# Performance work log

Hardware: AMD Instinct MI355X
Metric: run time of the kernel (lower is better)

## Reference

```python
import jax, jax.numpy as jnp
import numpy as np

N_NODES = 50000
N_EDGES = 400000
IN_DIM = 64
HID = 128
HEADS = 4
NEG_SLOPE = 0.2


def gat_conv(x, src, dst, W, a_src, a_dst, b, heads, out_ch, concat):
    N = x.shape[0]
    h = (x @ W).reshape(N, heads, out_ch)                 # [N,H,C]
    alpha_s = jnp.einsum('nhc,hc->nh', h, a_src)          # [N,H]
    alpha_d = jnp.einsum('nhc,hc->nh', h, a_dst)
    e = jax.nn.leaky_relu(alpha_s[src] + alpha_d[dst], NEG_SLOPE)  # [E,H]
    m = jax.ops.segment_max(e, dst, num_segments=N)
    m = jnp.where(jnp.isfinite(m), m, 0.0)
    ex = jnp.exp(e - m[dst])
    s = jax.ops.segment_sum(ex, dst, num_segments=N)
    alpha = ex / s[dst]                                   # segment softmax over incoming edges
    out = jax.ops.segment_sum(h[src] * alpha[:, :, None], dst, num_segments=N)  # [N,H,C]
    out = out.reshape(N, heads * out_ch) if concat else out.mean(axis=1)
    return out + b


def setup_inputs() -> dict:
    key = jax.random.key(0)
    ks = jax.random.split(key, 20)
    g = lambda i, shape, sc: (jax.random.normal(ks[i], shape, jnp.float32) * sc)
    x = g(0, (N_NODES, IN_DIM), 1.0)
    edge_index = jax.random.randint(ks[1], (2, N_EDGES), 0, N_NODES, dtype=jnp.int32)
    d = {
        'x': x, 'edge_index': edge_index,
        'W1': g(2, (IN_DIM, HEADS * HID), 0.1), 'a_src1': g(3, (HEADS, HID), 0.1), 'a_dst1': g(4, (HEADS, HID), 0.1), 'b1': jnp.zeros((HEADS * HID,), jnp.float32),
        'W2': g(5, (HEADS * HID, HEADS * HID), 0.05), 'a_src2': g(6, (HEADS, HID), 0.1), 'a_dst2': g(7, (HEADS, HID), 0.1), 'b2': jnp.zeros((HEADS * HID,), jnp.float32),
        'W3': g(8, (HEADS * HID, HID), 0.05), 'a_src3': g(9, (1, HID), 0.1), 'a_dst3': g(10, (1, HID), 0.1), 'b3': jnp.zeros((HID,), jnp.float32),
        'fc1_w': g(11, (HID, HID // 2), 0.1), 'fc1_b': jnp.zeros((HID // 2,), jnp.float32),
        'fc2_w': g(12, (HID // 2, 1), 0.1), 'fc2_b': jnp.zeros((1,), jnp.float32),
    }
    return d


def reference(x, edge_index, W1, a_src1, a_dst1, b1, W2, a_src2, a_dst2, b2, W3, a_src3, a_dst3, b3, fc1_w, fc1_b, fc2_w, fc2_b):
    N = x.shape[0]
    loop = jnp.arange(N, dtype=edge_index.dtype)
    src = jnp.concatenate([edge_index[0], loop])  # PyG GATConv adds self-loops by default
    dst = jnp.concatenate([edge_index[1], loop])
    h = jax.nn.elu(gat_conv(x, src, dst, W1, a_src1, a_dst1, b1, HEADS, HID, True))
    h = jax.nn.elu(gat_conv(h, src, dst, W2, a_src2, a_dst2, b2, HEADS, HID, True))
    h = jax.nn.elu(gat_conv(h, src, dst, W3, a_src3, a_dst3, b3, 1, HID, False))
    h = jax.nn.relu(h @ fc1_w + fc1_b)
    return jax.nn.sigmoid(h @ fc2_w + fc2_b)  # [N, 1]
```

## Files before the change

kernel.cpp:

```cpp
#include <hip/hip_runtime.h>
#include <math.h>

typedef __attribute__((ext_vector_type(8))) short short8;
typedef __attribute__((ext_vector_type(4))) float f32x4;
typedef unsigned short u16;
typedef unsigned int u32;

__device__ inline u16 f2b(float f) {
  u32 u = __float_as_uint(f);
  return (u16)((u + 0x7FFFu + ((u >> 16) & 1u)) >> 16);
}
__device__ inline float b2f(u16 b) { return __uint_as_float((u32)b << 16); }
__device__ inline float lrelu(float v) { return v > 0.f ? v : 0.2f * v; }
__device__ inline float elu1(float v) { return v > 0.f ? v : __expf(v) - 1.f; }

__device__ inline void gld_lds16(const void* g, void* l) {
  __builtin_amdgcn_global_load_lds((const __attribute__((address_space(1))) void*)g,
                                   (__attribute__((address_space(3))) void*)l, 16, 0, 0);
}

__global__ void fused_prep(const float* __restrict__ W1, u16* __restrict__ Wt1,
                           const float* __restrict__ W2, u16* __restrict__ Wt2,
                           const float* __restrict__ W3, u16* __restrict__ Wt3,
                           const int* __restrict__ ei, int E0, int ET,
                           int* __restrict__ deg) {
  int i = blockIdx.x * blockDim.x + threadIdx.x;
  if (i < 64 * 512) {
    int k = i / 512, n = i % 512;
    Wt1[n * 64 + k] = f2b(W1[i]);
    return;
  }
  i -= 64 * 512;
  if (i < 512 * 512) {
    int k = i / 512, n = i % 512;
    Wt2[n * 512 + k] = f2b(W2[i]);
    return;
  }
  i -= 512 * 512;
  if (i < 512 * 128) {
    int k = i / 128, n = i % 128;
    Wt3[n * 512 + k] = f2b(W3[i]);
    return;
  }
  i -= 512 * 128;
  if (i < ET) {
    int d = (i < E0) ? ei[E0 + i] : (i - E0);
    atomicAdd(&deg[d], 1);
  }
}

__global__ __launch_bounds__(256) void gemm_bf16_gat(
    const u16* __restrict__ A, const u16* __restrict__ Bt, u16* __restrict__ Hb,
    const float* __restrict__ a_src, const float* __restrict__ a_dst,
    float* __restrict__ aS, float* __restrict__ aD, int M, int HC, int K, int Hh,
    int gy, int nStrips) {
  int mIdx, nIdx;
  if (nStrips == 4) {
    int l = blockIdx.x;
    int xcd = l & 7, k = l >> 3;
    nIdx = k & 3;
    mIdx = xcd + 8 * (k >> 2);
    if (mIdx >= gy) return;
  } else {
    mIdx = blockIdx.x;
    nIdx = 0;
  }
  __shared__ u16 As[128 * 32];
  __shared__ u16 Bs[128 * 32];
  __shared__ float sRed[2][2][128];
  const int tid = threadIdx.x;
  const int w = tid >> 6, lane = tid & 63;
  const int wm = w >> 1, wn = w & 1;
  const int q = lane >> 4, l15 = lane & 15;
  const int nBase = nIdx * 128;
  const int mBase = mIdx * 128;
  const int h = nBase >> 7;
  const int srow = lane >> 2;
  const int skc = (lane & 3) * 8;

  f32x4 acc[4][4];
#pragma unroll
  for (int i = 0; i < 4; ++i)
#pragma unroll
    for (int j = 0; j < 4; ++j) acc[i][j] = (f32x4){0.f, 0.f, 0.f, 0.f};

  for (int k0 = 0; k0 < K; k0 += 32) {
#pragma unroll
    for (int r = 0; r < 2; ++r) {
      int lrow = w * 32 + r * 16 + srow;
      int ga = mBase + lrow;
      if (ga >= M) ga = M - 1;
      gld_lds16(A + (size_t)ga * K + k0 + skc, &As[(w * 32 + r * 16) * 32]);
      int gb = nBase + lrow;
      gld_lds16(Bt + (size_t)gb * K + k0 + skc, &Bs[(w * 32 + r * 16) * 32]);
    }
    __syncthreads();
    short8 af[4], bf[4];
#pragma unroll
    for (int i = 0; i < 4; ++i)
      af[i] = *(const short8*)&As[(wm * 64 + i * 16 + l15) * 32 + q * 8];
#pragma unroll
    for (int j = 0; j < 4; ++j)
      bf[j] = *(const short8*)&Bs[(wn * 64 + j * 16 + l15) * 32 + q * 8];
#pragma unroll
    for (int i = 0; i < 4; ++i)
#pragma unroll
      for (int j = 0; j < 4; ++j)
        acc[i][j] = __builtin_amdgcn_mfma_f32_16x16x32_bf16(af[i], bf[j], acc[i][j], 0, 0, 0);
    __syncthreads();
  }

  float asv[4], adv[4];
#pragma unroll
  for (int j = 0; j < 4; ++j) {
    int cw = wn * 64 + j * 16 + l15;
    asv[j] = a_src[h * 128 + cw];
    adv[j] = a_dst[h * 128 + cw];
  }
#pragma unroll
  for (int mi = 0; mi < 4; ++mi) {
#pragma unroll
    for (int r = 0; r < 4; ++r) {
      int row = mBase + wm * 64 + mi * 16 + q * 4 + r;
      float s = 0.f, d = 0.f;
#pragma unroll
      for (int j = 0; j < 4; ++j) {
        float v = acc[mi][j][r];
        s = fmaf(v, asv[j], s);
        d = fmaf(v, adv[j], d);
        if (row < M) Hb[(size_t)row * HC + nBase + wn * 64 + j * 16 + l15] = f2b(v);
      }
#pragma unroll
      for (int o = 8; o; o >>= 1) {
        s += __shfl_xor(s, o);
        d += __shfl_xor(d, o);
      }
      if (l15 == 0) {
        int lr = wm * 64 + mi * 16 + q * 4 + r;
        sRed[0][wn][lr] = s;
        sRed[1][wn][lr] = d;
      }
    }
  }
  __syncthreads();
  if (tid < 128) {
    int row = mBase + tid;
    if (row < M) {
      aS[(size_t)row * Hh + h] = sRed[0][0][tid] + sRed[0][1][tid];
      aD[(size_t)row * Hh + h] = sRed[1][0][tid] + sRed[1][1][tid];
    }
  }
}

__global__ __launch_bounds__(256) void gemm_bd_l1(
    const u16* __restrict__ A, const u16* __restrict__ Bt,
    const float* __restrict__ bias, u16* __restrict__ outB, int M, int gy) {
  int l = blockIdx.x;
  int xcd = l & 7, kk = l >> 3;
  int nIdx = kk & 3;
  int mIdx = xcd + 8 * (kk >> 2);
  if (mIdx >= gy) return;
  __shared__ u16 As[128 * 32];
  __shared__ u16 Bs[128 * 32];
  const int tid = threadIdx.x;
  const int w = tid >> 6, lane = tid & 63;
  const int wm = w >> 1, wn = w & 1;
  const int q = lane >> 4, l15 = lane & 15;
  const int nBase = nIdx * 128, mBase = mIdx * 128;
  const int srow = lane >> 2, skc = (lane & 3) * 8;

  f32x4 acc[4][4];
#pragma unroll
  for (int i = 0; i < 4; ++i)
#pragma unroll
    for (int j = 0; j < 4; ++j) acc[i][j] = (f32x4){0.f, 0.f, 0.f, 0.f};

  for (int k0 = 0; k0 < 64; k0 += 32) {
#pragma unroll
    for (int r = 0; r < 2; ++r) {
      int lrow = w * 32 + r * 16 + srow;
      int ga = mBase + lrow;
      if (ga >= M) ga = M - 1;
      gld_lds16(A + (size_t)ga * 256 + nIdx * 64 + k0 + skc,
                &As[(w * 32 + r * 16) * 32]);
      int gb = nBase + lrow;
      gld_lds16(Bt + (size_t)gb * 64 + k0 + skc, &Bs[(w * 32 + r * 16) * 32]);
    }
    __syncthreads();
    short8 af[4], bf[4];
#pragma unroll
    for (int i = 0; i < 4; ++i)
      af[i] = *(const short8*)&As[(wm * 64 + i * 16 + l15) * 32 + q * 8];
#pragma unroll
    for (int j = 0; j < 4; ++j)
      bf[j] = *(const short8*)&Bs[(wn * 64 + j * 16 + l15) * 32 + q * 8];
#pragma unroll
    for (int i = 0; i < 4; ++i)
#pragma unroll
      for (int j = 0; j < 4; ++j)
        acc[i][j] = __builtin_amdgcn_mfma_f32_16x16x32_bf16(af[i], bf[j], acc[i][j], 0, 0, 0);
    __syncthreads();
  }

  float bvv[4];
#pragma unroll
  for (int j = 0; j < 4; ++j) bvv[j] = bias[nBase + wn * 64 + j * 16 + l15];
#pragma unroll
  for (int mi = 0; mi < 4; ++mi)
#pragma unroll
    for (int r = 0; r < 4; ++r) {
      int row = mBase + wm * 64 + mi * 16 + q * 4 + r;
      if (row < M) {
#pragma unroll
        for (int j = 0; j < 4; ++j) {
          float v = elu1(acc[mi][j][r] + bvv[j]);
          outB[(size_t)row * 512 + nBase + wn * 64 + j * 16 + l15] = f2b(v);
        }
      }
    }
}

__global__ __launch_bounds__(256) void scan_chunk(const int* __restrict__ deg,
                                                  int* __restrict__ incl,
                                                  int* __restrict__ bsums, int N) {
  __shared__ int sdata[256];
  const int t = threadIdx.x;
  const int base = blockIdx.x * 2048;
  int v[8];
  int sum = 0;
#pragma unroll
  for (int i = 0; i < 8; ++i) {
    int idx = base + t * 8 + i;
    v[i] = (idx < N) ? deg[idx] : 0;
    sum += v[i];
  }
  sdata[t] = sum;
  __syncthreads();
  for (int off = 1; off < 256; off <<= 1) {
    int x = (t >= off) ? sdata[t - off] : 0;
    __syncthreads();
    sdata[t] += x;
    __syncthreads();
  }
  int run = (t > 0) ? sdata[t - 1] : 0;
#pragma unroll
  for (int i = 0; i < 8; ++i) {
    int idx = base + t * 8 + i;
    run += v[i];
    if (idx < N) incl[idx] = run;
  }
  if (t == 255) bsums[blockIdx.x] = sdata[255];
}

__global__ void scan_final(const int* __restrict__ incl, const int* __restrict__ bsums,
                           int* __restrict__ rowptr, int N, int nb) {
  int i = blockIdx.x * blockDim.x + threadIdx.x;
  if (i >= N) return;
  int chunk = i >> 11;
  int pre = 0;
  for (int j = 0; j < chunk; ++j) pre += bsums[j];
  rowptr[i + 1] = incl[i] + pre;
  if (i == 0) rowptr[0] = 0;
}

__global__ void csr_fill(const int* __restrict__ ei, int E0, int ET,
                         const int* __restrict__ rowptr, int* __restrict__ cnt,
                         int* __restrict__ csr_src, int* __restrict__ csr_dst) {
  int e = blockIdx.x * blockDim.x + threadIdx.x;
  if (e >= ET) return;
  int s, d;
  if (e < E0) { s = ei[e]; d = ei[E0 + e]; }
  else        { s = e - E0; d = e - E0; }
  int pos = atomicAdd(&cnt[d], 1);
  csr_src[rowptr[d] + pos] = s;
  csr_dst[rowptr[d] + pos] = d;
}

__global__ void make_wsd(const float* __restrict__ W1, const float* __restrict__ as1,
                         const float* __restrict__ ad1, float* __restrict__ wsd) {
  int t = blockIdx.x * blockDim.x + threadIdx.x;
  if (t >= 512) return;
  int k = t >> 3, c8 = t & 7;
  int h = c8 & 3;
  const float* a = (c8 >= 4) ? ad1 : as1;
  float s = 0.f;
  for (int c = 0; c < 128; ++c) s += W1[k * 512 + h * 128 + c] * a[h * 128 + c];
  wsd[k * 8 + c8] = s;
}

__global__ __launch_bounds__(256) void asad_x(const float* __restrict__ xf,
                                              const float* __restrict__ wsd,
                                              float* __restrict__ aS,
                                              float* __restrict__ aD, int N) {
  const int wid = (int)((blockIdx.x * (blockDim.x >> 6)) + (threadIdx.x >> 6));
  const int lane = threadIdx.x & 63;
  if (wid >= N) return;
  float xv = xf[(size_t)wid * 64 + lane];
  float4 w0 = *(const float4*)&wsd[lane * 8];
  float4 w1 = *(const float4*)&wsd[lane * 8 + 4];
  float s[8] = {xv * w0.x, xv * w0.y, xv * w0.z, xv * w0.w,
                xv * w1.x, xv * w1.y, xv * w1.z, xv * w1.w};
#pragma unroll
  for (int i = 0; i < 8; ++i)
#pragma unroll
    for (int o = 32; o; o >>= 1) s[i] += __shfl_xor(s[i], o);
  if (lane == 0) {
    *(float4*)&aS[(size_t)wid * 4] = make_float4(s[0], s[1], s[2], s[3]);
    *(float4*)&aD[(size_t)wid * 4] = make_float4(s[4], s[5], s[6], s[7]);
  }
}

__global__ __launch_bounds__(256) void edge_logits(const int* __restrict__ csr_src,
                                                   const int* __restrict__ csr_dst,
                                                   const float* __restrict__ aS,
                                                   const float* __restrict__ aD,
                                                   float* __restrict__ elog, int ET,
                                                   int Hh) {
  int e = blockIdx.x * blockDim.x + threadIdx.x;
  if (e >= ET) return;
  int s = csr_src[e], d = csr_dst[e];
  if (Hh == 4) {
    float4 a = *(const float4*)&aS[(size_t)s * 4];
    float4 b = *(const float4*)&aD[(size_t)d * 4];
    float4 r;
    r.x = lrelu(a.x + b.x);
    r.y = lrelu(a.y + b.y);
    r.z = lrelu(a.z + b.z);
    r.w = lrelu(a.w + b.w);
    *(float4*)&elog[(size_t)e * 4] = r;
  } else {
    elog[e] = lrelu(aS[s] + aD[d]);
  }
}

__global__ __launch_bounds__(256) void gat_agg_x(
    const int* __restrict__ rowptr, const int* __restrict__ csr_src,
    const float* __restrict__ xf, const float* __restrict__ elog,
    u16* __restrict__ aggB, int N) {
  const int wid = (int)((blockIdx.x * (blockDim.x >> 6)) + (threadIdx.x >> 6));
  const int lane = threadIdx.x & 63;
  if (wid >= N) return;
  const int beg = rowptr[wid];
  const int deg = rowptr[wid + 1] - beg;
  const int h = lane >> 4;
  const int e16 = lane & 15;
  float acc[4] = {};

  if (deg <= 16) {
    int srcv = 0;
    float l = -1e30f;
    if (e16 < deg) {
      srcv = csr_src[beg + e16];
      l = elog[(size_t)(beg + e16) * 4 + h];
    }
    float xv[16];
#pragma unroll
    for (int j = 0; j < 16; ++j)
      if (j < deg) {
        int s = __shfl(srcv, j);
        xv[j] = xf[(size_t)s * 64 + lane];
      }
    float m = l;
#pragma unroll
    for (int o = 8; o; o >>= 1) m = fmaxf(m, __shfl_xor(m, o));
    float pexp = (e16 < deg) ? __expf(l - m) : 0.f;
    float cs = pexp;
#pragma unroll
    for (int o = 8; o; o >>= 1) cs += __shfl_xor(cs, o);
    pexp *= (1.f / cs);
#pragma unroll
    for (int j = 0; j < 16; ++j)
      if (j < deg) {
        float w0 = __shfl(pexp, j);
        float w1 = __shfl(pexp, 16 | j);
        float w2 = __shfl(pexp, 32 | j);
        float w3 = __shfl(pexp, 48 | j);
        acc[0] = fmaf(w0, xv[j], acc[0]);
        acc[1] = fmaf(w1, xv[j], acc[1]);
        acc[2] = fmaf(w2, xv[j], acc[2]);
        acc[3] = fmaf(w3, xv[j], acc[3]);
      }
  } else {
    float m = -1e30f, ssum = 0.f;
    for (int c = 0; c < deg; c += 16) {
      const int ce = min(16, deg - c);
      int srcv = 0;
      float l = -1e30f;
      if (e16 < ce) {
        srcv = csr_src[beg + c + e16];
        l = elog[(size_t)(beg + c + e16) * 4 + h];
      }
      float xv[16];
#pragma unroll
      for (int j = 0; j < 16; ++j)
        if (j < ce) {
          int s = __shfl(srcv, j);
          xv[j] = xf[(size_t)s * 64 + lane];
        }
      float cm = l;
#pragma unroll
      for (int o = 8; o; o >>= 1) cm = fmaxf(cm, __shfl_xor(cm, o));
      float pexp, cs;
      if (c == 0) {
        m = cm;
        pexp = (e16 < ce) ? __expf(l - m) : 0.f;
        cs = pexp;
#pragma unroll
        for (int o = 8; o; o >>= 1) cs += __shfl_xor(cs, o);
        ssum = cs;
      } else {
        float newm = fmaxf(m, cm);
        float r = __expf(m - newm);
        m = newm;
        pexp = (e16 < ce) ? __expf(l - m) : 0.f;
        cs = pexp;
#pragma unroll
        for (int o = 8; o; o >>= 1) cs += __shfl_xor(cs, o);
        ssum = ssum * r + cs;
#pragma unroll
        for (int i = 0; i < 4; ++i) acc[i] *= r;
      }
#pragma unroll
      for (int j = 0; j < 16; ++j)
        if (j < ce) {
          float w0 = __shfl(pexp, j);
          float w1 = __shfl(pexp, 16 | j);
          float w2 = __shfl(pexp, 32 | j);
          float w3 = __shfl(pexp, 48 | j);
          acc[0] = fmaf(w0, xv[j], acc[0]);
          acc[1] = fmaf(w1, xv[j], acc[1]);
          acc[2] = fmaf(w2, xv[j], acc[2]);
          acc[3] = fmaf(w3, xv[j], acc[3]);
        }
    }
    const float inv = 1.f / ssum;
#pragma unroll
    for (int i = 0; i < 4; ++i) acc[i] *= inv;
  }
#pragma unroll
  for (int hh = 0; hh < 4; ++hh)
    aggB[((size_t)wid * 4 + hh) * 64 + lane] = f2b(acc[hh]);
}

#define ACC8(A, pv, wgt)                                             \
  A[0] = fmaf(wgt, __uint_as_float(pv.x << 16), A[0]);               \
  A[1] = fmaf(wgt, __uint_as_float(pv.x & 0xffff0000u), A[1]);       \
  A[2] = fmaf(wgt, __uint_as_float(pv.y << 16), A[2]);               \
  A[3] = fmaf(wgt, __uint_as_float(pv.y & 0xffff0000u), A[3]);       \
  A[4] = fmaf(wgt, __uint_as_float(pv.z << 16), A[4]);               \
  A[5] = fmaf(wgt, __uint_as_float(pv.z & 0xffff0000u), A[5]);       \
  A[6] = fmaf(wgt, __uint_as_float(pv.w << 16), A[6]);               \
  A[7] = fmaf(wgt, __uint_as_float(pv.w & 0xffff0000u), A[7]);

__global__ __launch_bounds__(256) void gat_fused_agg(
    const int* __restrict__ rowptr, const int* __restrict__ csr_src,
    const u16* __restrict__ Hb, const float* __restrict__ elog,
    const float* __restrict__ bias, u16* __restrict__ outB,
    float* __restrict__ outF, int N) {
  const int wid = (int)((blockIdx.x * (blockDim.x >> 6)) + (threadIdx.x >> 6));
  const int lane = threadIdx.x & 63;
  if (wid >= N) return;
  const int beg = rowptr[wid];
  const int deg = rowptr[wid + 1] - beg;

  const int h = lane >> 4;
  const int e16 = lane & 15;
  const int c0 = lane * 8;
  const int hbase = lane & 48;
  float acc[8] = {};

  if (deg <= 16) {
    int srcv = 0;
    float l = -1e30f;
    if (e16 < deg) {
      srcv = csr_src[beg + e16];
      l = elog[(size_t)(beg + e16) * 4 + h];
    }
    uint4 pC[4];
#pragma unroll
    for (int j = 0; j < 4; ++j)
      if (j < deg) {
        int s = __shfl(srcv, j);
        pC[j] = *(const uint4*)&Hb[(size_t)s * 512 + c0];
      }
    float m = l;
#pragma unroll
    for (int o = 8; o; o >>= 1) m = fmaxf(m, __shfl_xor(m, o));
    float pexp = (e16 < deg) ? __expf(l - m) : 0.f;
    float cs = pexp;
#pragma unroll
    for (int o = 8; o; o >>= 1) cs += __shfl_xor(cs, o);
    pexp *= (1.f / cs);
    int e = 0;
    for (; e + 4 < deg; e += 4) {
      uint4 pN[4];
      int rem = deg - e - 4;
#pragma unroll
      for (int j = 0; j < 4; ++j)
        if (j < rem) {
          int s = __shfl(srcv, e + 4 + j);
          pN[j] = *(const uint4*)&Hb[(size_t)s * 512 + c0];
        }
#pragma unroll
      for (int j = 0; j < 4; ++j) {
        float wgt = __shfl(pexp, hbase | (e + j));
        ACC8(acc, pC[j], wgt)
      }
#pragma unroll
      for (int j = 0; j < 4; ++j) pC[j] = pN[j];
    }
#pragma unroll
    for (int j = 0; j < 4; ++j)
      if (j < deg - e) {
        float wgt = __shfl(pexp, hbase | (e + j));
        ACC8(acc, pC[j], wgt)
      }
  } else {
    float m = -1e30f, ssum = 0.f;
    for (int c = 0; c < deg; c += 16) {
      const int ce = min(16, deg - c);
      int srcv = 0;
      float l = -1e30f;
      if (e16 < ce) {
        srcv = csr_src[beg + c + e16];
        l = elog[(size_t)(beg + c + e16) * 4 + h];
      }
      float cm = l;
#pragma unroll
      for (int o = 8; o; o >>= 1) cm = fmaxf(cm, __shfl_xor(cm, o));
      float pexp, cs;
      if (c == 0) {
        m = cm;
        pexp = __expf(l - m);
        cs = pexp;
#pragma unroll
        for (int o = 8; o; o >>= 1) cs += __shfl_xor(cs, o);
        ssum = cs;
      } else {
        float newm = fmaxf(m, cm);
        float r = __expf(m - newm);
        m = newm;
        pexp = __expf(l - m);
        cs = pexp;
#pragma unroll
        for (int o = 8; o; o >>= 1) cs += __shfl_xor(cs, o);
        ssum = ssum * r + cs;
#pragma unroll
        for (int i = 0; i < 8; ++i) acc[i] *= r;
      }
      int e = 0;
      for (; e + 4 <= ce; e += 4) {
        int se0 = __shfl(srcv, e + 0), se1 = __shfl(srcv, e + 1);
        int se2 = __shfl(srcv, e + 2), se3 = __shfl(srcv, e + 3);
        float w0 = __shfl(pexp, hbase | (e + 0)), w1 = __shfl(pexp, hbase | (e + 1));
        float w2 = __shfl(pexp, hbase | (e + 2)), w3 = __shfl(pexp, hbase | (e + 3));
        uint4 p0 = *(const uint4*)&Hb[(size_t)se0 * 512 + c0];
        uint4 p1 = *(const uint4*)&Hb[(size_t)se1 * 512 + c0];
        uint4 p2 = *(const uint4*)&Hb[(size_t)se2 * 512 + c0];
        uint4 p3 = *(const uint4*)&Hb[(size_t)se3 * 512 + c0];
        ACC8(acc, p0, w0)
        ACC8(acc, p1, w1)
        ACC8(acc, p2, w2)
        ACC8(acc, p3, w3)
      }
      for (; e < ce; ++e) {
        int se = __shfl(srcv, e);
        float wgt = __shfl(pexp, hbase | e);
        uint4 pv = *(const uint4*)&Hb[(size_t)se * 512 + c0];
        ACC8(acc, pv, wgt)
      }
    }
    const float inv = 1.f / ssum;
#pragma unroll
    for (int i = 0; i < 8; ++i) acc[i] *= inv;
  }

  float bv[8];
  *(float4*)&bv[0] = *(const float4*)&bias[c0];
  *(float4*)&bv[4] = *(const float4*)&bias[c0 + 4];
  u16 packed[8];
#pragma unroll
  for (int i = 0; i < 8; ++i) {
    float v = elu1(acc[i] + bv[i]);
    acc[i] = v;
    packed[i] = f2b(v);
  }
  if (outB) *(uint4*)&outB[(size_t)wid * 512 + c0] = *(const uint4*)packed;
  if (outF) {
    *(float4*)&outF[(size_t)wid * 512 + c0] = make_float4(acc[0], acc[1], acc[2], acc[3]);
    *(float4*)&outF[(size_t)wid * 512 + c0 + 4] =
        make_float4(acc[4], acc[5], acc[6], acc[7]);
  }
}

__global__ __launch_bounds__(256) void gat_agg_h1(
    const int* __restrict__ rowptr, const int* __restrict__ csr_src,
    const u16* __restrict__ Hb, const float* __restrict__ elog,
    const float* __restrict__ bias, float* __restrict__ outF, int N) {
  const int wid = (int)((blockIdx.x * (blockDim.x >> 6)) + (threadIdx.x >> 6));
  const int lane = threadIdx.x & 63;
  if (wid >= N) return;
  const int beg = rowptr[wid];
  const int deg = rowptr[wid + 1] - beg;
  const int g = lane & 15;
  const int es = lane >> 4;
  const int c0 = g * 8;
  float acc[8] = {};

  if (deg <= 64) {
    int srcv = 0;
    float l = -1e30f;
    if (lane < deg) {
      srcv = csr_src[beg + lane];
      l = elog[beg + lane];
    }
    const int dm1 = deg - 1;
    uint4 pC;
    {
      int s = __shfl(srcv, min(es, dm1));
      pC = *(const uint4*)&Hb[(size_t)s * 128 + c0];
    }
    float m = l;
#pragma unroll
    for (int o = 32; o; o >>= 1) m = fmaxf(m, __shfl_xor(m, o));
    float pexp = (lane < deg) ? __expf(l - m) : 0.f;
    float cs = pexp;
#pragma unroll
    for (int o = 32; o; o >>= 1) cs += __shfl_xor(cs, o);
    pexp *= (1.f / cs);
    int t = 0;
    for (; t + 4 < deg; t += 4) {
      uint4 pN;
      {
        int s = __shfl(srcv, min(t + 4 + es, dm1));
        pN = *(const uint4*)&Hb[(size_t)s * 128 + c0];
      }
      float w = __shfl(pexp, t + es);
      ACC8(acc, pC, w)
      pC = pN;
    }
    {
      int idx = t + es;
      float w = __shfl(pexp, min(idx, dm1));
      if (idx > dm1) w = 0.f;
      ACC8(acc, pC, w)
    }
  } else {
    float m = -1e30f, ssum = 0.f;
    for (int c = 0; c < deg; c += 64) {
      const int ce = min(64, deg - c);
      int srcv = 0;
      float l = -1e30f;
      if (lane < ce) {
        srcv = csr_src[beg + c + lane];
        l = elog[beg + c + lane];
      }
      float cm = l;
#pragma unroll
      for (int o = 32; o; o >>= 1) cm = fmaxf(cm, __shfl_xor(cm, o));
      float pexp, cs;
      if (c == 0) {
        m = cm;
        pexp = __expf(l - m);
        cs = pexp;
#pragma unroll
        for (int o = 32; o; o >>= 1) cs += __shfl_xor(cs, o);
        ssum = cs;
      } else {
        float newm = fmaxf(m, cm);
        float r = __expf(m - newm);
        m = newm;
        pexp = __expf(l - m);
        cs = pexp;
#pragma unroll
        for (int o = 32; o; o >>= 1) cs += __shfl_xor(cs, o);
        ssum = ssum * r + cs;
#pragma unroll
        for (int i = 0; i < 8; ++i) acc[i] *= r;
      }
      for (int t = 0; t < ce; t += 4) {
        int idx = t + es;
        int se = __shfl(srcv, idx & 63);
        float wgt = __shfl(pexp, idx & 63);
        if (idx < ce) {
          uint4 pv = *(const uint4*)&Hb[(size_t)se * 128 + c0];
          ACC8(acc, pv, wgt)
        }
      }
    }
    const float inv = 1.f / ssum;
#pragma unroll
    for (int i = 0; i < 8; ++i) acc[i] *= inv;
  }
#pragma unroll
  for (int i = 0; i < 8; ++i) {
    acc[i] += __shfl_xor(acc[i], 16);
    acc[i] += __shfl_xor(acc[i], 32);
  }
  if (lane < 16) {
    float o[8];
#pragma unroll
    for (int i = 0; i < 8; ++i) o[i] = elu1(acc[i] + bias[c0 + i]);
    *(float4*)&outF[(size_t)wid * 128 + c0] = make_float4(o[0], o[1], o[2], o[3]);
    *(float4*)&outF[(size_t)wid * 128 + c0 + 4] = make_float4(o[4], o[5], o[6], o[7]);
  }
}

__global__ __launch_bounds__(256) void fc_head(const float* __restrict__ A,
                                               const float* __restrict__ B,
                                               const float* __restrict__ bias,
                                               const float* __restrict__ w2,
                                               const float* __restrict__ b2,
                                               float* __restrict__ out, int M) {
  __shared__ float As[16][64];
  __shared__ float Bs[16][64];
  __shared__ float sP[64][17];
  const int tid = threadIdx.x;
  const int tx = tid & 15, ty = tid >> 4;
  const int mBase = blockIdx.y * 64;
  const int aRow = tid >> 2;
  const int aK = (tid & 3) << 2;
  const int bC = tid & 63;
  const int bR0 = tid >> 6;
  const int K = 128, N = 64;
  float acc[4][4] = {};
  for (int k0 = 0; k0 < K; k0 += 16) {
    float4 av = make_float4(0.f, 0.f, 0.f, 0.f);
    int gr = mBase + aRow;
    if (gr < M) av = *(const float4*)&A[(size_t)gr * K + k0 + aK];
    As[aK + 0][aRow] = av.x;
    As[aK + 1][aRow] = av.y;
    As[aK + 2][aRow] = av.z;
    As[aK + 3][aRow] = av.w;
#pragma unroll
    for (int i = 0; i < 4; ++i) {
      int r = bR0 + i * 4;
      Bs[r][bC] = B[(size_t)(k0 + r) * N + bC];
    }
    __syncthreads();
#pragma unroll
    for (int k = 0; k < 16; ++k) {
      float4 a = *(const float4*)&As[k][ty * 4];
      float4 b = *(const float4*)&Bs[k][tx * 4];
      float ar[4] = {a.x, a.y, a.z, a.w};
      float br[4] = {b.x, b.y, b.z, b.w};
#pragma unroll
      for (int i = 0; i < 4; ++i)
#pragma unroll
        for (int j = 0; j < 4; ++j) acc[i][j] = fmaf(ar[i], br[j], acc[i][j]);
    }
    __syncthreads();
  }
  float4 bv = *(const float4*)&bias[tx * 4];
  float4 wv = *(const float4*)&w2[tx * 4];
#pragma unroll
  for (int i = 0; i < 4; ++i) {
    float p = 0.f;
    p = fmaf(fmaxf(acc[i][0] + bv.x, 0.f), wv.x, p);
    p = fmaf(fmaxf(acc[i][1] + bv.y, 0.f), wv.y, p);
    p = fmaf(fmaxf(acc[i][2] + bv.z, 0.f), wv.z, p);
    p = fmaf(fmaxf(acc[i][3] + bv.w, 0.f), wv.w, p);
    sP[ty * 4 + i][tx] = p;
  }
  __syncthreads();
  if (tid < 64) {
    int row = mBase + tid;
    if (row < M) {
      float s = 0.f;
#pragma unroll
      for (int t = 0; t < 16; ++t) s += sP[tid][t];
      out[row] = 1.f / (1.f + expf(-(s + b2[0])));
    }
  }
}

extern "C" void kernel_launch(void* const* d_in, const int* in_sizes, int n_in,
                              void* d_out, int out_size, void* d_ws, size_t ws_size,
                              hipStream_t stream) {
  const float* x    = (const float*)d_in[0];
  const int*   ei   = (const int*)d_in[1];
  const float* W1   = (const float*)d_in[2];
  const float* as1  = (const float*)d_in[3];
  const float* ad1  = (const float*)d_in[4];
  const float* b1   = (const float*)d_in[5];
  const float* W2   = (const float*)d_in[6];
  const float* as2  = (const float*)d_in[7];
  const float* ad2  = (const float*)d_in[8];
  const float* b2   = (const float*)d_in[9];
  const float* W3   = (const float*)d_in[10];
  const float* as3  = (const float*)d_in[11];
  const float* ad3  = (const float*)d_in[12];
  const float* b3   = (const float*)d_in[13];
  const float* fc1w = (const float*)d_in[14];
  const float* fc1b = (const float*)d_in[15];
  const float* fc2w = (const float*)d_in[16];
  const float* fc2b = (const float*)d_in[17];
  float* out = (float*)d_out;

  const int N  = in_sizes[0] / 64;
  const int E0 = in_sizes[1] / 2;
  const int ET = E0 + N;

  char* ws = (char*)d_ws;
  size_t off = 0;
  auto alloc = [&](size_t bytes) -> void* {
    void* p = ws + off;
    off += (bytes + 255) & ~(size_t)255;
    return p;
  };
  u16*   bufXb   = (u16*)alloc((size_t)N * 512 * 2);
  u16*   bufHb   = (u16*)alloc((size_t)N * 512 * 2);
  float* bufF    = (float*)alloc((size_t)N * 128 * 4);
  float* aS      = (float*)alloc((size_t)N * 4 * 4);
  float* aD      = (float*)alloc((size_t)N * 4 * 4);
  u16*   Wt1     = (u16*)alloc((size_t)512 * 64 * 2);
  u16*   Wt2     = (u16*)alloc((size_t)512 * 512 * 2);
  u16*   Wt3     = (u16*)alloc((size_t)128 * 512 * 2);
  u16*   aggB    = (u16*)alloc((size_t)N * 256 * 2);
  float* wsd     = (float*)alloc((size_t)64 * 8 * 4);
  int*   degcnt  = (int*)alloc((size_t)2 * N * 4);
  int*   deg     = degcnt;
  int*   cnt     = degcnt + N;
  int*   incl    = (int*)alloc((size_t)N * 4);
  int*   rowptr  = (int*)alloc((size_t)(N + 1) * 4);
  int*   bsums   = (int*)alloc(256 * 4);
  int*   csr_src = (int*)alloc((size_t)ET * 4);
  int*   csr_dst = (int*)alloc((size_t)ET * 4);
  float* elog    = (float*)alloc((size_t)ET * 4 * 4);
  (void)ws_size; (void)n_in; (void)out_size;

  hipMemsetAsync(degcnt, 0, (size_t)2 * N * 4, stream);
  const int prepTotal = 64 * 512 + 512 * 512 + 512 * 128 + ET;
  hipLaunchKernelGGL(fused_prep, dim3((prepTotal + 255) / 256), dim3(256), 0, stream,
                     W1, Wt1, W2, Wt2, W3, Wt3, ei, E0, ET, deg);

  int nb = (N + 2047) / 2048;
  hipLaunchKernelGGL(scan_chunk, dim3(nb), dim3(256), 0, stream, deg, incl, bsums, N);
  hipLaunchKernelGGL(scan_final, dim3((N + 255) / 256), dim3(256), 0, stream, incl, bsums,
                     rowptr, N, nb);
  int eb = (ET + 255) / 256;
  hipLaunchKernelGGL(csr_fill, dim3(eb), dim3(256), 0, stream, ei, E0, ET, rowptr, cnt,
                     csr_src, csr_dst);

  const int gy = (N + 127) / 128;
  const int grid4 = ((gy + 7) / 8) * 8 * 4;
  const int aggGrid = (N + 3) / 4;

  hipLaunchKernelGGL(make_wsd, dim3(2), dim3(256), 0, stream, W1, as1, ad1, wsd);
  hipLaunchKernelGGL(asad_x, dim3(aggGrid), dim3(256), 0, stream, x, wsd, aS, aD, N);
  hipLaunchKernelGGL(edge_logits, dim3(eb), dim3(256), 0, stream, csr_src, csr_dst, aS,
                     aD, elog, ET, 4);
  hipLaunchKernelGGL(gat_agg_x, dim3(aggGrid), dim3(256), 0, stream, rowptr, csr_src, x,
                     elog, aggB, N);
  hipLaunchKernelGGL(gemm_bd_l1, dim3(grid4), dim3(256), 0, stream, aggB, Wt1, b1,
                     bufXb, N, gy);

  hipLaunchKernelGGL(gemm_bf16_gat, dim3(grid4), dim3(256), 0, stream, bufXb, Wt2, bufHb,
                     as2, ad2, aS, aD, N, 512, 512, 4, gy, 4);
  hipLaunchKernelGGL(edge_logits, dim3(eb), dim3(256), 0, stream, csr_src, csr_dst, aS,
                     aD, elog, ET, 4);
  hipLaunchKernelGGL(gat_fused_agg, dim3(aggGrid), dim3(256), 0, stream, rowptr,
                     csr_src, bufHb, elog, b2, bufXb, nullptr, N);

  hipLaunchKernelGGL(gemm_bf16_gat, dim3(gy), dim3(256), 0, stream, bufXb, Wt3, bufHb,
                     as3, ad3, aS, aD, N, 128, 512, 1, gy, 1);
  hipLaunchKernelGGL(edge_logits, dim3(eb), dim3(256), 0, stream, csr_src, csr_dst, aS,
                     aD, elog, ET, 1);
  hipLaunchKernelGGL(gat_agg_h1, dim3(aggGrid), dim3(256), 0, stream, rowptr, csr_src,
                     bufHb, elog, b3, bufF, N);

  hipLaunchKernelGGL(fc_head, dim3(1, (N + 63) / 64), dim3(256), 0, stream, bufF, fc1w,
                     fc1b, fc2w, fc2b, out, N);
}
```

Before: 454.4 us.

## Double-buffer LDS tiles and XOR-swizzle layout in bf16 GEMM kernels

Both GEMM kernels now use two LDS buffers, so the global-to-LDS load of the next K slice is issued before the MFMA work on the current slice, overlapping memory latency with compute. The LDS layout is also XOR-swizzled on write and read to reduce bank conflicts on the short8 fragment loads. This doubles LDS use per block, which may lower occupancy. There is no wait between issuing the async loads and the barrier beyond __syncthreads, so correctness depends on the barrier also draining the global_load_lds operations.

Result: no change. 451.2 us (-0.7%).

```diff
diff --git a/kernel.cpp b/kernel.cpp
--- a/kernel.cpp
+++ b/kernel.cpp
@@ -65,8 +65,8 @@
     mIdx = blockIdx.x;
     nIdx = 0;
   }
-  __shared__ u16 As[128 * 32];
-  __shared__ u16 Bs[128 * 32];
+  __shared__ u16 As[2][128 * 32];
+  __shared__ u16 Bs[2][128 * 32];
   __shared__ float sRed[2][2][128];
   const int tid = threadIdx.x;
   const int w = tid >> 6, lane = tid & 63;
@@ -76,7 +76,8 @@
   const int mBase = mIdx * 128;
   const int h = nBase >> 7;
   const int srow = lane >> 2;
-  const int skc = (lane & 3) * 8;
+  const int ssw = ((lane & 3) ^ ((lane >> 3) & 3)) * 8;
+  const int rq = (q ^ ((l15 >> 1) & 3)) * 8;
 
   f32x4 acc[4][4];
 #pragma unroll
@@ -84,30 +85,45 @@
 #pragma unroll
     for (int j = 0; j < 4; ++j) acc[i][j] = (f32x4){0.f, 0.f, 0.f, 0.f};
 
-  for (int k0 = 0; k0 < K; k0 += 32) {
-#pragma unroll
-    for (int r = 0; r < 2; ++r) {
-      int lrow = w * 32 + r * 16 + srow;
-      int ga = mBase + lrow;
-      if (ga >= M) ga = M - 1;
-      gld_lds16(A + (size_t)ga * K + k0 + skc, &As[(w * 32 + r * 16) * 32]);
-      int gb = nBase + lrow;
-      gld_lds16(Bt + (size_t)gb * K + k0 + skc, &Bs[(w * 32 + r * 16) * 32]);
-    }
-    __syncthreads();
+  const int nSteps = K >> 5;
+#pragma unroll
+  for (int r = 0; r < 2; ++r) {
+    int lrow0 = w * 32 + r * 16;
+    int ga = mBase + lrow0 + srow;
+    if (ga >= M) ga = M - 1;
+    gld_lds16(A + (size_t)ga * K + ssw, &As[0][lrow0 * 32]);
+    int gb = nBase + lrow0 + srow;
+    gld_lds16(Bt + (size_t)gb * K + ssw, &Bs[0][lrow0 * 32]);
+  }
+  __syncthreads();
+  int cur = 0;
+  for (int step = 0; step < nSteps; ++step) {
+    const int k0n = (step + 1) << 5;
+    if (k0n < K) {
+#pragma unroll
+      for (int r = 0; r < 2; ++r) {
+        int lrow0 = w * 32 + r * 16;
+        int ga = mBase + lrow0 + srow;
+        if (ga >= M) ga = M - 1;
+        gld_lds16(A + (size_t)ga * K + k0n + ssw, &As[cur ^ 1][lrow0 * 32]);
+        int gb = nBase + lrow0 + srow;
+        gld_lds16(Bt + (size_t)gb * K + k0n + ssw, &Bs[cur ^ 1][lrow0 * 32]);
+      }
+    }
     short8 af[4], bf[4];
 #pragma unroll
     for (int i = 0; i < 4; ++i)
-      af[i] = *(const short8*)&As[(wm * 64 + i * 16 + l15) * 32 + q * 8];
+      af[i] = *(const short8*)&As[cur][(wm * 64 + i * 16 + l15) * 32 + rq];
 #pragma unroll
     for (int j = 0; j < 4; ++j)
-      bf[j] = *(const short8*)&Bs[(wn * 64 + j * 16 + l15) * 32 + q * 8];
+      bf[j] = *(const short8*)&Bs[cur][(wn * 64 + j * 16 + l15) * 32 + rq];
 #pragma unroll
     for (int i = 0; i < 4; ++i)
 #pragma unroll
       for (int j = 0; j < 4; ++j)
         acc[i][j] = __builtin_amdgcn_mfma_f32_16x16x32_bf16(af[i], bf[j], acc[i][j], 0, 0, 0);
     __syncthreads();
+    cur ^= 1;
   }
 
   float asv[4], adv[4];
@@ -160,14 +176,16 @@
   int nIdx = kk & 3;
   int mIdx = xcd + 8 * (kk >> 2);
   if (mIdx >= gy) return;
-  __shared__ u16 As[128 * 32];
-  __shared__ u16 Bs[128 * 32];
+  __shared__ u16 As[2][128 * 32];
+  __shared__ u16 Bs[2][128 * 32];
   const int tid = threadIdx.x;
   const int w = tid >> 6, lane = tid & 63;
   const int wm = w >> 1, wn = w & 1;
   const int q = lane >> 4, l15 = lane & 15;
   const int nBase = nIdx * 128, mBase = mIdx * 128;
-  const int srow = lane >> 2, skc = (lane & 3) * 8;
+  const int srow = lane >> 2;
+  const int ssw = ((lane & 3) ^ ((lane >> 3) & 3)) * 8;
+  const int rq = (q ^ ((l15 >> 1) & 3)) * 8;
 
   f32x4 acc[4][4];
 #pragma unroll
@@ -175,31 +193,44 @@
 #pragma unroll
     for (int j = 0; j < 4; ++j) acc[i][j] = (f32x4){0.f, 0.f, 0.f, 0.f};
 
-  for (int k0 = 0; k0 < 64; k0 += 32) {
-#pragma unroll
-    for (int r = 0; r < 2; ++r) {
-      int lrow = w * 32 + r * 16 + srow;
-      int ga = mBase + lrow;
-      if (ga >= M) ga = M - 1;
-      gld_lds16(A + (size_t)ga * 256 + nIdx * 64 + k0 + skc,
-                &As[(w * 32 + r * 16) * 32]);
-      int gb = nBase + lrow;
-      gld_lds16(Bt + (size_t)gb * 64 + k0 + skc, &Bs[(w * 32 + r * 16) * 32]);
-    }
-    __syncthreads();
+#pragma unroll
+  for (int r = 0; r < 2; ++r) {
+    int lrow0 = w * 32 + r * 16;
+    int ga = mBase + lrow0 + srow;
+    if (ga >= M) ga = M - 1;
+    gld_lds16(A + (size_t)ga * 256 + nIdx * 64 + ssw, &As[0][lrow0 * 32]);
+    int gb = nBase + lrow0 + srow;
+    gld_lds16(Bt + (size_t)gb * 64 + ssw, &Bs[0][lrow0 * 32]);
+  }
+  __syncthreads();
+  int cur = 0;
+#pragma unroll
+  for (int step = 0; step < 2; ++step) {
+    if (step == 0) {
+#pragma unroll
+      for (int r = 0; r < 2; ++r) {
+        int lrow0 = w * 32 + r * 16;
+        int ga = mBase + lrow0 + srow;
+        if (ga >= M) ga = M - 1;
+        gld_lds16(A + (size_t)ga * 256 + nIdx * 64 + 32 + ssw, &As[1][lrow0 * 32]);
+        int gb = nBase + lrow0 + srow;
+        gld_lds16(Bt + (size_t)gb * 64 + 32 + ssw, &Bs[1][lrow0 * 32]);
+      }
+    }
     short8 af[4], bf[4];
 #pragma unroll
     for (int i = 0; i < 4; ++i)
-      af[i] = *(const short8*)&As[(wm * 64 + i * 16 + l15) * 32 + q * 8];
+      af[i] = *(const short8*)&As[cur][(wm * 64 + i * 16 + l15) * 32 + rq];
 #pragma unroll
     for (int j = 0; j < 4; ++j)
-      bf[j] = *(const short8*)&Bs[(wn * 64 + j * 16 + l15) * 32 + q * 8];
+      bf[j] = *(const short8*)&Bs[cur][(wn * 64 + j * 16 + l15) * 32 + rq];
 #pragma unroll
     for (int i = 0; i < 4; ++i)
 #pragma unroll
       for (int j = 0; j < 4; ++j)
         acc[i][j] = __builtin_amdgcn_mfma_f32_16x16x32_bf16(af[i], bf[j], acc[i][j], 0, 0, 0);
     __syncthreads();
+    cur ^= 1;
   }
 
   float bvv[4];
```
